# Kernel optimization log

Hardware: AMD Instinct MI355X
Metric: run time of the kernel (lower is better)

## Reference

```python
import jax, jax.numpy as jnp
import numpy as np

N, A, C = 4, 8732, 81
SCALE_XY, SCALE_WH = 0.1, 0.2   # dboxes.scale_xy / scale_wh; Loss uses reciprocals
LAM, W_IOU = 1.0, 0.01
EPS_IOU = float(np.finfo(float).eps)


def setup_inputs() -> dict:
    key = jax.random.key(0)
    ks = jax.random.split(key, 8)
    ploc = jax.random.normal(ks[0], (N, 4, A), dtype=jnp.float32) * 0.5
    plabel = jax.random.normal(ks[1], (N, C, A), dtype=jnp.float32)
    # ground-truth loc in xywh with strictly positive wh (loc_vec takes a log)
    gxy = jax.random.uniform(ks[2], (N, 2, A), dtype=jnp.float32)
    gwh = jax.random.uniform(ks[3], (N, 2, A), dtype=jnp.float32) * 0.4 + 0.05
    gloc = jnp.concatenate([gxy, gwh], axis=1)
    lab = jax.random.randint(ks[4], (N, A), 1, C)
    keep = jax.random.uniform(ks[5], (N, A)) < 0.02
    glabel = jnp.where(keep, lab, 0).astype(jnp.int32)
    # default boxes in xywh, shape [1, 4, A]
    dxy = jax.random.uniform(ks[6], (1, 2, A), dtype=jnp.float32)
    dwh = jax.random.uniform(ks[7], (1, 2, A), dtype=jnp.float32) * 0.45 + 0.05
    dboxes = jnp.concatenate([dxy, dwh], axis=1)
    return {"ploc": ploc, "plabel": plabel, "gloc": gloc, "glabel": glabel, "dboxes": dboxes}


def _decode_ltrb(loc, dboxes):
    """scale_back_batch: encoded [N,4,A] + dboxes xywh [1,4,A] -> ltrb [N,A,4]."""
    b = jnp.transpose(loc, (0, 2, 1))      # [N, A, 4]
    d = jnp.transpose(dboxes, (0, 2, 1))   # [1, A, 4]
    xy = SCALE_XY * b[..., :2] * d[..., 2:] + d[..., :2]
    wh = jnp.exp(SCALE_WH * b[..., 2:]) * d[..., 2:]
    return jnp.concatenate([xy - 0.5 * wh, xy + 0.5 * wh], axis=-1)


def _iou_sum(p, g):
    """p, g: [A,4] ltrb -> per-anchor sum over all g boxes of IoU(p_i, g_k)."""
    area_p = (p[:, 2] - p[:, 0]) * (p[:, 3] - p[:, 1])
    area_g = (g[:, 2] - g[:, 0]) * (g[:, 3] - g[:, 1])
    iw = jnp.maximum(jnp.minimum(p[:, None, 2], g[None, :, 2]) - jnp.maximum(p[:, None, 0], g[None, :, 0]), 0.0)
    ih = jnp.maximum(jnp.minimum(p[:, None, 3], g[None, :, 3]) - jnp.maximum(p[:, None, 1], g[None, :, 1]), 0.0)
    inter = iw * ih                                      # [A, A]
    ua = jnp.maximum(area_p[:, None] + area_g[None, :] - inter, EPS_IOU)
    return (inter / ua).sum(axis=1)                      # [A]


def _forward(ploc, plabel, gloc, glabel, dboxes):
    mask = glabel > 0                                    # [N, A]
    pos_num = mask.sum(axis=1)                           # [N]

    # loc_vec: encode ground truth against default boxes
    dxy, dwh = dboxes[:, :2, :], dboxes[:, 2:, :]
    gxy_t = (1.0 / SCALE_XY) * (gloc[:, :2, :] - dxy) / dwh
    gwh_t = (1.0 / SCALE_WH) * jnp.log(gloc[:, 2:, :] / dwh)
    vec_gd = jnp.concatenate([gxy_t, gwh_t], axis=1)     # [N, 4, A]

    # SmoothL1 (beta=1), summed over coord dim
    diff = ploc - vec_gd
    ad = jnp.abs(diff)
    sl1 = jnp.where(ad < 1.0, 0.5 * diff * diff, ad - 0.5).sum(axis=1)  # [N, A]

    # per-anchor cross entropy
    logp = jax.nn.log_softmax(plabel, axis=1)            # [N, C, A]
    con = -jnp.take_along_axis(logp, glabel[:, None, :], axis=1)[:, 0, :]  # [N, A]

    # weighted-IoU reweighting (weights are detached in the original)
    p_ltrb = _decode_ltrb(ploc, dboxes)                  # [N, A, 4]
    g_ltrb = _decode_ltrb(gloc, dboxes)
    iou_s = jax.vmap(_iou_sum)(p_ltrb, g_ltrb)           # [N, A]
    valid = (p_ltrb[..., 0] < p_ltrb[..., 2]) & (p_ltrb[..., 1] < p_ltrb[..., 3])
    weights = jnp.where(valid, W_IOU * iou_s ** LAM, 0.0)
    weights = jax.lax.stop_gradient(weights)
    sl1 = (sl1 / (sl1 + weights)) * sl1

    sl1_pos = (mask.astype(sl1.dtype) * sl1).sum(axis=1)  # [N]

    # hard negative mining: double argsort for ranks
    con_neg = jnp.where(mask, 0.0, con)
    con_idx = jnp.argsort(-con_neg, axis=1)
    con_rank = jnp.argsort(con_idx, axis=1)
    neg_num = jnp.minimum(3 * pos_num, A)[:, None]
    neg_mask = con_rank < neg_num
    closs = (con * (mask.astype(con.dtype) + neg_mask.astype(con.dtype))).sum(axis=1)

    total = sl1_pos + closs
    num_mask = (pos_num > 0).astype(total.dtype)
    pn = jnp.maximum(pos_num.astype(total.dtype), 1e-6)
    return (total * num_mask / pn).mean()


def reference(ploc, plabel, gloc, glabel, dboxes):
    return _forward(ploc, plabel, gloc, glabel, dboxes)
```

## Files before the change

### kernel.cpp

```cpp
#include <hip/hip_runtime.h>
#include <math.h>

#define A_N 8732
#define NAT (4 * A_N)
#define BATCH 4
#define CLS 81
#define TILE 256
#define ABLK 35
#define NBINS 2048
#define PLB 128

__device__ __forceinline__ float sl1f(float d) {
    float ad = fabsf(d);
    return ad < 1.0f ? 0.5f * d * d : ad - 0.5f;
}
__device__ __forceinline__ unsigned umap(float v) {
    return __float_as_uint(v) | 0x80000000u;
}

__device__ void suffix_find(const int* lcnt, const float* lsum, int k, int tid,
                            int* ic, float* fsum,
                            int* o_b, int* o_krem, float* o_sumA)
{
    int base = tid * 8;
    int cs = 0; float ss = 0.0f;
    #pragma unroll
    for (int j = 0; j < 8; j++) { cs += lcnt[base + j]; ss += lsum[base + j]; }
    ic[tid] = cs; fsum[tid] = ss;
    __syncthreads();
    for (int off = 1; off < TILE; off <<= 1) {
        int v = ic[tid]; float f = fsum[tid];
        int v2 = 0; float f2 = 0.0f;
        if (tid + off < TILE) { v2 = ic[tid + off]; f2 = fsum[tid + off]; }
        __syncthreads();
        ic[tid] = v + v2; fsum[tid] = f + f2;
        __syncthreads();
    }
    int run = ic[tid] - cs;
    float runs = fsum[tid] - ss;
    for (int j = 7; j >= 0; j--) {
        int b = base + j; int c = lcnt[b];
        if (run < k && run + c >= k) { *o_b = b; *o_krem = k - run; *o_sumA = runs; }
        run += c; runs += lsum[b];
    }
    __syncthreads();
}

__global__ __launch_bounds__(TILE) void prep_kernel(
    const float* __restrict__ ploc, const float* __restrict__ plabel,
    const float* __restrict__ gloc, const int* __restrict__ glabel,
    const float* __restrict__ dboxes,
    float4* __restrict__ pbox, float4* __restrict__ gbox,
    float* __restrict__ sl1raw, float* __restrict__ conneg,
    int* __restrict__ poslist,
    int* __restrict__ poscnt,
    float* __restrict__ consum)
{
    __shared__ int   wcnt[4];
    __shared__ float wsum[4];
    const int tid = threadIdx.x;
    const int blk = blockIdx.x;
    const int a = blk * TILE + tid;
    const int n = blockIdx.y;

    bool msk = false;
    float cv = 0.0f;
    if (a < A_N) {
        const float* pb = plabel + (size_t)n * CLS * A_N + a;
        float se = 0.0f;
        #pragma unroll 27
        for (int c = 0; c < CLS; c++) se += expf(pb[(size_t)c * A_N]);
        int lab = glabel[n * A_N + a];
        float xg = pb[(size_t)lab * A_N];
        cv = logf(se) - xg;
        msk = lab > 0;
        conneg[n * A_N + a] = msk ? 0.0f : cv;

        float d0 = dboxes[0*A_N+a], d1 = dboxes[1*A_N+a], d2 = dboxes[2*A_N+a], d3 = dboxes[3*A_N+a];
        const float* pl = ploc + (size_t)n * 4 * A_N;
        const float* gl = gloc + (size_t)n * 4 * A_N;
        float p0 = pl[0*A_N+a], p1 = pl[1*A_N+a], p2 = pl[2*A_N+a], p3 = pl[3*A_N+a];
        float g0 = gl[0*A_N+a], g1 = gl[1*A_N+a], g2 = gl[2*A_N+a], g3 = gl[3*A_N+a];

        float v0 = 10.0f * (g0 - d0) / d2;
        float v1 = 10.0f * (g1 - d1) / d3;
        float v2 = 5.0f * logf(g2 / d2);
        float v3 = 5.0f * logf(g3 / d3);
        sl1raw[n * A_N + a] = sl1f(p0-v0) + sl1f(p1-v1) + sl1f(p2-v2) + sl1f(p3-v3);

        float cx = 0.1f*p0*d2 + d0, cy = 0.1f*p1*d3 + d1;
        float cw = expf(0.2f*p2)*d2, ch = expf(0.2f*p3)*d3;
        pbox[(size_t)n*A_N + a] = make_float4(cx-0.5f*cw, cy-0.5f*ch, cx+0.5f*cw, cy+0.5f*ch);
        float ex = 0.1f*g0*d2 + d0, ey = 0.1f*g1*d3 + d1;
        float ew = expf(0.2f*g2)*d2, eh = expf(0.2f*g3)*d3;
        gbox[(size_t)n*A_N + a] = make_float4(ex-0.5f*ew, ey-0.5f*eh, ex+0.5f*ew, ey+0.5f*eh);
    }

    unsigned long long bal = __ballot(msk);
    int wid = tid >> 6, lane = tid & 63;
    float wv = msk ? cv : 0.0f;
    #pragma unroll
    for (int off = 32; off > 0; off >>= 1) wv += __shfl_down(wv, off);
    if (lane == 0) { wcnt[wid] = __popcll(bal); wsum[wid] = wv; }
    __syncthreads();
    if (msk) {
        int base = 0;
        for (int w = 0; w < wid; w++) base += wcnt[w];
        int off = base + (int)__popcll(bal & ((1ULL << lane) - 1ULL));
        poslist[(n * ABLK + blk) * TILE + off] = a;
    }
    if (tid == 0) {
        poscnt[n * ABLK + blk] = wcnt[0] + wcnt[1] + wcnt[2] + wcnt[3];
        consum[n * ABLK + blk] = wsum[0] + wsum[1] + wsum[2] + wsum[3];
    }
}

__global__ __launch_bounds__(TILE) void tail_kernel(
    const float4* __restrict__ pbox, const float4* __restrict__ gbox,
    const float* __restrict__ sl1raw, const float* __restrict__ conneg,
    const int* __restrict__ poslist, const int* __restrict__ poscnt,
    const float* __restrict__ consum,
    float* __restrict__ out)
{
    __shared__ int   spre[ABLK + 1];
    __shared__ float r4[4];
    const int n = blockIdx.y, tid = threadIdx.x;

    if (tid == 0) {
        int run = 0;
        #pragma unroll
        for (int s = 0; s < ABLK; s++) { spre[s] = run; run += poscnt[n * ABLK + s]; }
        spre[ABLK] = run;
    }
    __syncthreads();
    const int np = spre[ABLK];
    if (np <= 0) return;
    const float inv = 1.0f / ((float)np * (float)BATCH);

    if (blockIdx.x < PLB) {
        for (int p = blockIdx.x; p < np; p += PLB) {
            int s = 0;
            while (spre[s + 1] <= p) s++;
            int a = poslist[(n * ABLK + s) * TILE + (p - spre[s])];
            float4 b = pbox[(size_t)n * A_N + a];
            float ap = (b.z - b.x) * (b.w - b.y);
            float acc = 0.0f;
            for (int k = tid; k < A_N; k += TILE) {
                float4 g = gbox[(size_t)n * A_N + k];
                float iw = fmaxf(fminf(b.z, g.z) - fmaxf(b.x, g.x), 0.0f);
                float ih = fmaxf(fminf(b.w, g.w) - fmaxf(b.y, g.y), 0.0f);
                float inter = iw * ih;
                float ua = ap + (g.z - g.x) * (g.w - g.y) - inter;
                acc += inter * __builtin_amdgcn_rcpf(ua);
            }
            #pragma unroll
            for (int off = 32; off > 0; off >>= 1) acc += __shfl_down(acc, off);
            if ((tid & 63) == 0) r4[tid >> 6] = acc;
            __syncthreads();
            if (tid == 0) {
                float iou = r4[0] + r4[1] + r4[2] + r4[3];
                bool valid = (b.x < b.z) && (b.y < b.w);
                float w = valid ? 0.01f * iou : 0.0f;
                float sv = sl1raw[n * A_N + a];
                atomicAdd(out, (sv / (sv + w) * sv) * inv);
            }
            __syncthreads();
        }
    } else {
        __shared__ int   lcnt[NBINS];
        __shared__ float lsum[NBINS];
        __shared__ int   ic[TILE];
        __shared__ float fs_[TILE];
        __shared__ int sb1, skrem1, sb2, skrem2;
        __shared__ float ssA1, ssA2;
        int k = min(3 * np, A_N);

        for (int b = tid; b < NBINS; b += TILE) { lcnt[b] = 0; lsum[b] = 0.0f; }
        __syncthreads();
        for (int i = tid; i < A_N; i += TILE) {
            float v = conneg[n * A_N + i];
            int d = (umap(v) >> 20) & (NBINS - 1);
            atomicAdd(&lcnt[d], 1);
            atomicAdd(&lsum[d], v);
        }
        __syncthreads();
        suffix_find(lcnt, lsum, k, tid, ic, fs_, &sb1, &skrem1, &ssA1);
        int b1 = sb1;
        __syncthreads();

        for (int b = tid; b < NBINS; b += TILE) { lcnt[b] = 0; lsum[b] = 0.0f; }
        __syncthreads();
        for (int i = tid; i < A_N; i += TILE) {
            float v = conneg[n * A_N + i];
            unsigned u = umap(v);
            if ((int)((u >> 20) & (NBINS - 1)) == b1) {
                int d = (u >> 9) & (NBINS - 1);
                atomicAdd(&lcnt[d], 1);
                atomicAdd(&lsum[d], v);
            }
        }
        __syncthreads();
        suffix_find(lcnt, lsum, skrem1, tid, ic, fs_, &sb2, &skrem2, &ssA2);

        if (tid == 0) {
            float conpos = 0.0f;
            #pragma unroll
            for (int s = 0; s < ABLK; s++) conpos += consum[n * ABLK + s];
            unsigned ubin = 0x80000000u | ((unsigned)sb1 << 20) | ((unsigned)sb2 << 9) | 256u;
            float tval = __uint_as_float(ubin & 0x7fffffffu);
            float closs_neg = ssA1 + ssA2 + (float)skrem2 * tval;
            atomicAdd(out, (conpos + closs_neg) * inv);
        }
    }
}

extern "C" void kernel_launch(void* const* d_in, const int* in_sizes, int n_in,
                              void* d_out, int out_size, void* d_ws, size_t ws_size,
                              hipStream_t stream) {
    const float* ploc   = (const float*)d_in[0];
    const float* plabel = (const float*)d_in[1];
    const float* gloc   = (const float*)d_in[2];
    const int*   glabel = (const int*)d_in[3];
    const float* dboxes = (const float*)d_in[4];
    float* out = (float*)d_out;

    float4* pbox    = (float4*)d_ws;
    float4* gbox    = pbox + NAT;
    float*  sl1raw  = (float*)(gbox + NAT);
    float*  conneg  = sl1raw + NAT;
    int*    poslist = (int*)(conneg + NAT);
    int*    poscnt  = poslist + BATCH * ABLK * TILE;
    float*  consum  = (float*)(poscnt + BATCH * ABLK);

    hipMemsetAsync(d_out, 0, sizeof(float), stream);
    prep_kernel<<<dim3(ABLK, BATCH), TILE, 0, stream>>>(
        ploc, plabel, gloc, glabel, dboxes,
        pbox, gbox, sl1raw, conneg, poslist, poscnt, consum);
    tail_kernel<<<dim3(PLB + 1, BATCH), TILE, 0, stream>>>(
        pbox, gbox, sl1raw, conneg, poslist, poscnt, consum, out);
}
```

Measured before the change: 100.7 us.

## Split class logsumexp across four thread chunks, vectorize histogram, drop memset

The prep kernel now runs 512-thread blocks of 128 anchors each, and four thread groups each sum exp over about 20 classes. The partial sums and the label logit are combined through shared memory, which gives four times more memory-level parallelism on the plabel reads, the dominant traffic. The tail histogram passes read conneg as float4, and the output zeroing moves from a separate memset into the prep kernel. Three-quarters of the threads sit idle during the box and ballot phase, and the histogram float4 loop drops the tail elements if A_N is not divisible by 4 (8732 is divisible).

```diff
diff --git a/kernel.cpp b/kernel.cpp
--- a/kernel.cpp
+++ b/kernel.cpp
@@ -6,7 +6,9 @@
 #define BATCH 4
 #define CLS 81
 #define TILE 256
-#define ABLK 35
+#define PTHREADS 512
+#define SEG 128
+#define ABLKP 69
 #define NBINS 2048
 #define PLB 128
 
@@ -46,7 +48,7 @@
     __syncthreads();
 }
 
-__global__ __launch_bounds__(TILE) void prep_kernel(
+__global__ __launch_bounds__(PTHREADS) void prep_kernel(
     const float* __restrict__ ploc, const float* __restrict__ plabel,
     const float* __restrict__ gloc, const int* __restrict__ glabel,
     const float* __restrict__ dboxes,
@@ -54,25 +56,46 @@
     float* __restrict__ sl1raw, float* __restrict__ conneg,
     int* __restrict__ poslist,
     int* __restrict__ poscnt,
-    float* __restrict__ consum)
+    float* __restrict__ consum,
+    float* __restrict__ out)
 {
-    __shared__ int   wcnt[4];
-    __shared__ float wsum[4];
-    const int tid = threadIdx.x;
+    __shared__ float sh_se[4][SEG];
+    __shared__ float sh_xg[4][SEG];
+    __shared__ int   wcnt[2];
+    __shared__ float wsum[2];
+    const int t   = threadIdx.x;
     const int blk = blockIdx.x;
-    const int a = blk * TILE + tid;
-    const int n = blockIdx.y;
+    const int n   = blockIdx.y;
+    const int i     = t & (SEG - 1);
+    const int chunk = t >> 7;
+    const int a = blk * SEG + i;
+
+    if (t == 0 && blk == 0 && n == 0) *out = 0.0f;
+
+    int lab = 0;
+    float se = 0.0f, xv = 0.0f;
+    if (a < A_N) {
+        lab = glabel[n * A_N + a];
+        const float* pb = plabel + (size_t)n * CLS * A_N + a;
+        const int c0 = chunk * 20 + (chunk > 0 ? 1 : 0);
+        const int c1 = c0 + (chunk == 0 ? 21 : 20);
+        #pragma unroll 21
+        for (int c = c0; c < c1; c++) {
+            float x = pb[(size_t)c * A_N];
+            se += expf(x);
+            xv = (c == lab) ? x : xv;
+        }
+    }
+    sh_se[chunk][i] = se;
+    sh_xg[chunk][i] = xv;
+    __syncthreads();
 
     bool msk = false;
     float cv = 0.0f;
-    if (a < A_N) {
-        const float* pb = plabel + (size_t)n * CLS * A_N + a;
-        float se = 0.0f;
-        #pragma unroll 27
-        for (int c = 0; c < CLS; c++) se += expf(pb[(size_t)c * A_N]);
-        int lab = glabel[n * A_N + a];
-        float xg = pb[(size_t)lab * A_N];
-        cv = logf(se) - xg;
+    if (t < SEG && a < A_N) {
+        float set = sh_se[0][i] + sh_se[1][i] + sh_se[2][i] + sh_se[3][i];
+        float xg  = sh_xg[0][i] + sh_xg[1][i] + sh_xg[2][i] + sh_xg[3][i];
+        cv = logf(set) - xg;
         msk = lab > 0;
         conneg[n * A_N + a] = msk ? 0.0f : cv;
 
@@ -97,21 +120,20 @@
     }
 
     unsigned long long bal = __ballot(msk);
-    int wid = tid >> 6, lane = tid & 63;
+    int wid = t >> 6, lane = t & 63;
     float wv = msk ? cv : 0.0f;
     #pragma unroll
     for (int off = 32; off > 0; off >>= 1) wv += __shfl_down(wv, off);
-    if (lane == 0) { wcnt[wid] = __popcll(bal); wsum[wid] = wv; }
+    if (t < SEG && lane == 0) { wcnt[wid] = __popcll(bal); wsum[wid] = wv; }
     __syncthreads();
     if (msk) {
-        int base = 0;
-        for (int w = 0; w < wid; w++) base += wcnt[w];
+        int base = (wid == 1) ? wcnt[0] : 0;
         int off = base + (int)__popcll(bal & ((1ULL << lane) - 1ULL));
-        poslist[(n * ABLK + blk) * TILE + off] = a;
-    }
-    if (tid == 0) {
-        poscnt[n * ABLK + blk] = wcnt[0] + wcnt[1] + wcnt[2] + wcnt[3];
-        consum[n * ABLK + blk] = wsum[0] + wsum[1] + wsum[2] + wsum[3];
+        poslist[(n * ABLKP + blk) * SEG + off] = a;
+    }
+    if (t == 0) {
+        poscnt[n * ABLKP + blk] = wcnt[0] + wcnt[1];
+        consum[n * ABLKP + blk] = wsum[0] + wsum[1];
     }
 }
 
@@ -122,18 +144,18 @@
     const float* __restrict__ consum,
     float* __restrict__ out)
 {
-    __shared__ int   spre[ABLK + 1];
+    __shared__ int   spre[ABLKP + 1];
     __shared__ float r4[4];
     const int n = blockIdx.y, tid = threadIdx.x;
 
     if (tid == 0) {
         int run = 0;
         #pragma unroll
-        for (int s = 0; s < ABLK; s++) { spre[s] = run; run += poscnt[n * ABLK + s]; }
-        spre[ABLK] = run;
-    }
-    __syncthreads();
-    const int np = spre[ABLK];
+        for (int s = 0; s < ABLKP; s++) { spre[s] = run; run += poscnt[n * ABLKP + s]; }
+        spre[ABLKP] = run;
+    }
+    __syncthreads();
+    const int np = spre[ABLKP];
     if (np <= 0) return;
     const float inv = 1.0f / ((float)np * (float)BATCH);
 
@@ -141,7 +163,7 @@
         for (int p = blockIdx.x; p < np; p += PLB) {
             int s = 0;
             while (spre[s + 1] <= p) s++;
-            int a = poslist[(n * ABLK + s) * TILE + (p - spre[s])];
+            int a = poslist[(n * ABLKP + s) * SEG + (p - spre[s])];
             float4 b = pbox[(size_t)n * A_N + a];
             float ap = (b.z - b.x) * (b.w - b.y);
             float acc = 0.0f;
@@ -175,13 +197,19 @@
         __shared__ float ssA1, ssA2;
         int k = min(3 * np, A_N);
 
+        const float4* cn4 = (const float4*)(conneg + (size_t)n * A_N);
+
         for (int b = tid; b < NBINS; b += TILE) { lcnt[b] = 0; lsum[b] = 0.0f; }
         __syncthreads();
-        for (int i = tid; i < A_N; i += TILE) {
-            float v = conneg[n * A_N + i];
-            int d = (umap(v) >> 20) & (NBINS - 1);
-            atomicAdd(&lcnt[d], 1);
-            atomicAdd(&lsum[d], v);
+        for (int i = tid; i < A_N / 4; i += TILE) {
+            float4 v = cn4[i];
+            #pragma unroll
+            for (int j = 0; j < 4; j++) {
+                float vv = (j == 0) ? v.x : (j == 1) ? v.y : (j == 2) ? v.z : v.w;
+                int d = (umap(vv) >> 20) & (NBINS - 1);
+                atomicAdd(&lcnt[d], 1);
+                atomicAdd(&lsum[d], vv);
+            }
         }
         __syncthreads();
         suffix_find(lcnt, lsum, k, tid, ic, fs_, &sb1, &skrem1, &ssA1);
@@ -190,13 +218,17 @@
 
         for (int b = tid; b < NBINS; b += TILE) { lcnt[b] = 0; lsum[b] = 0.0f; }
         __syncthreads();
-        for (int i = tid; i < A_N; i += TILE) {
-            float v = conneg[n * A_N + i];
-            unsigned u = umap(v);
-            if ((int)((u >> 20) & (NBINS - 1)) == b1) {
-                int d = (u >> 9) & (NBINS - 1);
-                atomicAdd(&lcnt[d], 1);
-                atomicAdd(&lsum[d], v);
+        for (int i = tid; i < A_N / 4; i += TILE) {
+            float4 v = cn4[i];
+            #pragma unroll
+            for (int j = 0; j < 4; j++) {
+                float vv = (j == 0) ? v.x : (j == 1) ? v.y : (j == 2) ? v.z : v.w;
+                unsigned u = umap(vv);
+                if ((int)((u >> 20) & (NBINS - 1)) == b1) {
+                    int d = (u >> 9) & (NBINS - 1);
+                    atomicAdd(&lcnt[d], 1);
+                    atomicAdd(&lsum[d], vv);
+                }
             }
         }
         __syncthreads();
@@ -205,7 +237,7 @@
         if (tid == 0) {
             float conpos = 0.0f;
             #pragma unroll
-            for (int s = 0; s < ABLK; s++) conpos += consum[n * ABLK + s];
+            for (int s = 0; s < ABLKP; s++) conpos += consum[n * ABLKP + s];
             unsigned ubin = 0x80000000u | ((unsigned)sb1 << 20) | ((unsigned)sb2 << 9) | 256u;
             float tval = __uint_as_float(ubin & 0x7fffffffu);
             float closs_neg = ssA1 + ssA2 + (float)skrem2 * tval;
@@ -229,13 +261,12 @@
     float*  sl1raw  = (float*)(gbox + NAT);
     float*  conneg  = sl1raw + NAT;
     int*    poslist = (int*)(conneg + NAT);
-    int*    poscnt  = poslist + BATCH * ABLK * TILE;
-    float*  consum  = (float*)(poscnt + BATCH * ABLK);
-
-    hipMemsetAsync(d_out, 0, sizeof(float), stream);
-    prep_kernel<<<dim3(ABLK, BATCH), TILE, 0, stream>>>(
+    int*    poscnt  = poslist + BATCH * ABLKP * SEG;
+    float*  consum  = (float*)(poscnt + BATCH * ABLKP);
+
+    prep_kernel<<<dim3(ABLKP, BATCH), PTHREADS, 0, stream>>>(
         ploc, plabel, gloc, glabel, dboxes,
-        pbox, gbox, sl1raw, conneg, poslist, poscnt, consum);
+        pbox, gbox, sl1raw, conneg, poslist, poscnt, consum, out);
     tail_kernel<<<dim3(PLB + 1, BATCH), TILE, 0, stream>>>(
         pbox, gbox, sl1raw, conneg, poslist, poscnt, consum, out);
 }
```

Measured after the change: 105.4 us. +4.7%, slower.

## Use wave-shuffle scans, cache conneg in LDS, and fold output zeroing into prep

Applied to the files above, without the earlier changes.

The block-wide Hillis-Steele scan in suffix_find, which needed two barriers per step, is replaced by a wave shuffle scan plus a small cross-wave combine. The radix-select block now loads conneg into LDS once with float4 reads and reuses it in the second pass instead of reading global memory again. The hipMemsetAsync on the output is removed and the zeroing moved into prep_kernel, saving one launch. The poscnt and consum reductions are parallelized across threads. A cost is larger LDS use (about 35KB more) in the tail kernel, which may lower occupancy for the IoU blocks that share the kernel.

```diff
diff --git a/kernel.cpp b/kernel.cpp
--- a/kernel.cpp
+++ b/kernel.cpp
@@ -18,30 +18,31 @@
     return __float_as_uint(v) | 0x80000000u;
 }
 
-__device__ void suffix_find(const int* lcnt, const float* lsum, int k, int tid,
-                            int* ic, float* fsum,
-                            int* o_b, int* o_krem, float* o_sumA)
+__device__ __forceinline__ void suffix_find(const int* lcnt, const float* lsum,
+        int k, int tid, int* wtc, float* wts,
+        int* o_b, int* o_krem, float* o_sumA)
 {
-    int base = tid * 8;
+    const int base = tid * 8;
     int cs = 0; float ss = 0.0f;
     #pragma unroll
     for (int j = 0; j < 8; j++) { cs += lcnt[base + j]; ss += lsum[base + j]; }
-    ic[tid] = cs; fsum[tid] = ss;
-    __syncthreads();
-    for (int off = 1; off < TILE; off <<= 1) {
-        int v = ic[tid]; float f = fsum[tid];
-        int v2 = 0; float f2 = 0.0f;
-        if (tid + off < TILE) { v2 = ic[tid + off]; f2 = fsum[tid + off]; }
-        __syncthreads();
-        ic[tid] = v + v2; fsum[tid] = f + f2;
-        __syncthreads();
-    }
-    int run = ic[tid] - cs;
-    float runs = fsum[tid] - ss;
+    int c = cs; float s = ss;
+    const int lane = tid & 63;
+    #pragma unroll
+    for (int off = 1; off < 64; off <<= 1) {
+        int c2 = __shfl_down(c, off); float s2 = __shfl_down(s, off);
+        if (lane + off < 64) { c += c2; s += s2; }
+    }
+    const int wid = tid >> 6;
+    if (lane == 0) { wtc[wid] = c; wts[wid] = s; }
+    __syncthreads();
+    int run = c - cs; float runs = s - ss;
+    #pragma unroll
+    for (int w = 0; w < 4; w++) if (w > wid) { run += wtc[w]; runs += wts[w]; }
     for (int j = 7; j >= 0; j--) {
-        int b = base + j; int c = lcnt[b];
-        if (run < k && run + c >= k) { *o_b = b; *o_krem = k - run; *o_sumA = runs; }
-        run += c; runs += lsum[b];
+        int b = base + j; int cb = lcnt[b];
+        if (run < k && run + cb >= k) { *o_b = b; *o_krem = k - run; *o_sumA = runs; }
+        run += cb; runs += lsum[b];
     }
     __syncthreads();
 }
@@ -54,7 +55,8 @@
     float* __restrict__ sl1raw, float* __restrict__ conneg,
     int* __restrict__ poslist,
     int* __restrict__ poscnt,
-    float* __restrict__ consum)
+    float* __restrict__ consum,
+    float* __restrict__ out)
 {
     __shared__ int   wcnt[4];
     __shared__ float wsum[4];
@@ -62,6 +64,8 @@
     const int blk = blockIdx.x;
     const int a = blk * TILE + tid;
     const int n = blockIdx.y;
+
+    if (tid == 0 && blk == 0 && n == 0) *out = 0.0f;
 
     bool msk = false;
     float cv = 0.0f;
@@ -123,13 +127,16 @@
     float* __restrict__ out)
 {
     __shared__ int   spre[ABLK + 1];
+    __shared__ int   pv_[ABLK];
     __shared__ float r4[4];
     const int n = blockIdx.y, tid = threadIdx.x;
 
+    if (tid < ABLK) pv_[tid] = poscnt[n * ABLK + tid];
+    __syncthreads();
     if (tid == 0) {
         int run = 0;
         #pragma unroll
-        for (int s = 0; s < ABLK; s++) { spre[s] = run; run += poscnt[n * ABLK + s]; }
+        for (int s = 0; s < ABLK; s++) { spre[s] = run; run += pv_[s]; }
         spre[ABLK] = run;
     }
     __syncthreads();
@@ -167,45 +174,58 @@
             __syncthreads();
         }
     } else {
+        __shared__ float cnv[A_N];
         __shared__ int   lcnt[NBINS];
         __shared__ float lsum[NBINS];
-        __shared__ int   ic[TILE];
-        __shared__ float fs_[TILE];
+        __shared__ int   wtc[4];
+        __shared__ float wts[4];
         __shared__ int sb1, skrem1, sb2, skrem2;
         __shared__ float ssA1, ssA2;
         int k = min(3 * np, A_N);
 
+        const float4* cn4 = (const float4*)(conneg + (size_t)n * A_N);
+        float4* cnv4 = (float4*)cnv;
+
         for (int b = tid; b < NBINS; b += TILE) { lcnt[b] = 0; lsum[b] = 0.0f; }
         __syncthreads();
+        for (int i = tid; i < A_N / 4; i += TILE) {
+            float4 v = cn4[i];
+            cnv4[i] = v;
+            #pragma unroll
+            for (int j = 0; j < 4; j++) {
+                float vv = (j == 0) ? v.x : (j == 1) ? v.y : (j == 2) ? v.z : v.w;
+                int d = (umap(vv) >> 20) & (NBINS - 1);
+                atomicAdd(&lcnt[d], 1);
+                atomicAdd(&lsum[d], vv);
+            }
+        }
+        __syncthreads();
+        suffix_find(lcnt, lsum, k, tid, wtc, wts, &sb1, &skrem1, &ssA1);
+        int b1 = sb1;
+        __syncthreads();
+
+        for (int b = tid; b < NBINS; b += TILE) { lcnt[b] = 0; lsum[b] = 0.0f; }
+        __syncthreads();
         for (int i = tid; i < A_N; i += TILE) {
-            float v = conneg[n * A_N + i];
-            int d = (umap(v) >> 20) & (NBINS - 1);
-            atomicAdd(&lcnt[d], 1);
-            atomicAdd(&lsum[d], v);
-        }
-        __syncthreads();
-        suffix_find(lcnt, lsum, k, tid, ic, fs_, &sb1, &skrem1, &ssA1);
-        int b1 = sb1;
-        __syncthreads();
-
-        for (int b = tid; b < NBINS; b += TILE) { lcnt[b] = 0; lsum[b] = 0.0f; }
-        __syncthreads();
-        for (int i = tid; i < A_N; i += TILE) {
-            float v = conneg[n * A_N + i];
-            unsigned u = umap(v);
+            float vv = cnv[i];
+            unsigned u = umap(vv);
             if ((int)((u >> 20) & (NBINS - 1)) == b1) {
                 int d = (u >> 9) & (NBINS - 1);
                 atomicAdd(&lcnt[d], 1);
-                atomicAdd(&lsum[d], v);
-            }
-        }
-        __syncthreads();
-        suffix_find(lcnt, lsum, skrem1, tid, ic, fs_, &sb2, &skrem2, &ssA2);
-
+                atomicAdd(&lsum[d], vv);
+            }
+        }
+        __syncthreads();
+        suffix_find(lcnt, lsum, skrem1, tid, wtc, wts, &sb2, &skrem2, &ssA2);
+
+        float cp = 0.0f;
+        if (tid < ABLK) cp = consum[n * ABLK + tid];
+        #pragma unroll
+        for (int off = 32; off > 0; off >>= 1) cp += __shfl_down(cp, off);
+        if ((tid & 63) == 0) r4[tid >> 6] = cp;
+        __syncthreads();
         if (tid == 0) {
-            float conpos = 0.0f;
-            #pragma unroll
-            for (int s = 0; s < ABLK; s++) conpos += consum[n * ABLK + s];
+            float conpos = r4[0] + r4[1] + r4[2] + r4[3];
             unsigned ubin = 0x80000000u | ((unsigned)sb1 << 20) | ((unsigned)sb2 << 9) | 256u;
             float tval = __uint_as_float(ubin & 0x7fffffffu);
             float closs_neg = ssA1 + ssA2 + (float)skrem2 * tval;
@@ -232,10 +252,9 @@
     int*    poscnt  = poslist + BATCH * ABLK * TILE;
     float*  consum  = (float*)(poscnt + BATCH * ABLK);
 
-    hipMemsetAsync(d_out, 0, sizeof(float), stream);
     prep_kernel<<<dim3(ABLK, BATCH), TILE, 0, stream>>>(
         ploc, plabel, gloc, glabel, dboxes,
-        pbox, gbox, sl1raw, conneg, poslist, poscnt, consum);
+        pbox, gbox, sl1raw, conneg, poslist, poscnt, consum, out);
     tail_kernel<<<dim3(PLB + 1, BATCH), TILE, 0, stream>>>(
         pbox, gbox, sl1raw, conneg, poslist, poscnt, consum, out);
 }
```

After: 99.58 us. Within noise of the previous version (-1.1%).
